# Kernel tuning notes

Hardware: AMD Instinct MI355X
Metric: run time of the kernel (lower is better)

Reference implementation:

```python
import jax, jax.numpy as jnp
import numpy as np

N_ENT = 100000
EMBED_DIM = 128
N_EDGES = 3200000
SPARSE_THRESHOLD = 5


def setup_inputs() -> dict:
    key = jax.random.key(0)
    k1, k2, k3, k4 = jax.random.split(key, 4)
    entity_embeds = jax.random.normal(k1, (N_ENT, EMBED_DIM), dtype=jnp.float32)
    node_degrees = jax.random.randint(k2, (N_ENT,), 0, 40, dtype=jnp.int64)
    path_rows = jnp.sort(jax.random.randint(k3, (N_EDGES,), 0, N_ENT, dtype=jnp.int64))
    path_cols = jax.random.randint(k4, (N_EDGES,), 0, N_ENT, dtype=jnp.int64)
    return {
        "entity_embeds": entity_embeds,
        "node_degrees": node_degrees,
        "path_rows": path_rows,
        "path_cols": path_cols,
    }


def reference(entity_embeds, node_degrees, path_rows, path_cols):
    N, dim = entity_embeds.shape
    # node_edge_count = scatter_add(ones, rows), clamped to >= 1
    ones = jnp.ones(path_rows.shape[0], dtype=entity_embeds.dtype)
    node_edge_count = jax.ops.segment_sum(ones, path_rows, num_segments=N)
    node_edge_count = jnp.clip(node_edge_count, 1.0, None)
    # SpMM: remote[i] = sum over path edges (i -> j) of entity_embeds[j]
    gathered = entity_embeds[path_cols]  # [E, dim] (fused into segment_sum by XLA)
    remote = jax.ops.segment_sum(gathered, path_rows, num_segments=N)
    # degree-normalize then mask to sparse (low-degree) nodes only
    remote = remote / node_edge_count[:, None]
    sparse_mask = (node_degrees <= SPARSE_THRESHOLD).astype(entity_embeds.dtype)
    remote = remote * sparse_mask[:, None]
    return remote
```

## Files before the change

kernel.cpp:

```cpp
#include <hip/hip_runtime.h>

#define N_ENT 100000
#define EMBED_DIM 128
#define SPARSE_THRESHOLD 5
#define N4 (N_ENT * 32)

#define WS_ROWSTART_OFF 64
#define WS_LIST_OFF     100096
#define WS_BF16_OFF_INT 200096
#define WS_NEEDED_BYTES ((size_t)WS_BF16_OFF_INT * 4 + (size_t)N4 * 8)

#define B_ZERO 1408
#define B_CONV 2304
#define B_BND  352
#define B_CMP  32
#define B_TOT  (B_ZERO + B_CONV + B_BND + B_CMP)

__device__ __forceinline__ unsigned short bf16_rne(float f) {
    unsigned int u = __float_as_uint(f);
    u += 0x7FFFu + ((u >> 16) & 1u);
    return (unsigned short)(u >> 16);
}
__device__ __forceinline__ float bf16_up(unsigned short h) {
    return __uint_as_float(((unsigned int)h) << 16);
}

__global__ __launch_bounds__(256) void prep_kernel(
    const float4* __restrict__ emb4,
    const int*    __restrict__ rows,
    const int*    __restrict__ degrees,
    float4*       __restrict__ out4,
    ushort4*      __restrict__ embw,
    int*          __restrict__ row_start,
    int*          __restrict__ sparse_list,
    int*          __restrict__ counter,
    int n_edges)
{
    const int b = blockIdx.x;
    if (b < B_ZERO) {
        const float4 z = make_float4(0.f, 0.f, 0.f, 0.f);
        for (int i = b * 256 + threadIdx.x; i < N4; i += B_ZERO * 256)
            out4[i] = z;
    } else if (b < B_ZERO + B_CONV) {
        for (int i = (b - B_ZERO) * 256 + threadIdx.x; i < N4; i += B_CONV * 256) {
            const float4 v = emb4[i];
            ushort4 o;
            o.x = bf16_rne(v.x); o.y = bf16_rne(v.y);
            o.z = bf16_rne(v.z); o.w = bf16_rne(v.w);
            embw[i] = o;
        }
    } else if (b < B_ZERO + B_CONV + B_BND) {
        const int t  = (b - B_ZERO - B_CONV) * 256 + threadIdx.x;
        const int NT = B_BND * 256;
        const int4* rows4 = (const int4*)rows;
        const int n_quads = n_edges >> 2;
        for (int q = t; q < n_quads; q += NT) {
            const int e0 = q << 2;
            const int4 v = rows4[q];
            int rp = (e0 == 0) ? -1 : rows[e0 - 1];
            const int rv[4] = {v.x, v.y, v.z, v.w};
            #pragma unroll
            for (int k = 0; k < 4; ++k) {
                const int e = e0 + k;
                const int r = rv[k];
                for (int qq = rp + 1; qq <= r; ++qq) row_start[qq] = e;
                if (e == n_edges - 1)
                    for (int qq = r + 1; qq <= N_ENT; ++qq) row_start[qq] = n_edges;
                rp = r;
            }
        }
        for (int e = (n_quads << 2) + t; e < n_edges; e += NT) {
            const int r  = rows[e];
            const int rp = (e == 0) ? -1 : rows[e - 1];
            for (int qq = rp + 1; qq <= r; ++qq) row_start[qq] = e;
            if (e == n_edges - 1)
                for (int qq = r + 1; qq <= N_ENT; ++qq) row_start[qq] = n_edges;
        }
    } else {
        const int t = (b - B_ZERO - B_CONV - B_BND) * 256 + threadIdx.x;
        for (int r = t; r < N_ENT; r += B_CMP * 256) {
            if (degrees[r] <= SPARSE_THRESHOLD)
                sparse_list[atomicAdd(counter, 1)] = r;
        }
    }
}

__global__ __launch_bounds__(256) void agg_sparse_bf16_kernel(
    const ushort4* __restrict__ embw,
    const int*     __restrict__ row_start,
    const int*     __restrict__ cols,
    const int*     __restrict__ sparse_list,
    const int*     __restrict__ counter,
    float4*        __restrict__ out4)
{
    const int nsparse = *counter;
    const int sub  = threadIdx.x >> 5;
    const int lane = threadIdx.x & 31;

    for (int idx = blockIdx.x * 8 + sub; idx < nsparse; idx += gridDim.x * 8) {
        const int row   = sparse_list[idx];
        const int start = row_start[row];
        const int end   = row_start[row + 1];

        float4 acc = make_float4(0.f, 0.f, 0.f, 0.f);
        int e = start;
        for (; e + 8 <= end; e += 8) {
            int c[8];
            #pragma unroll
            for (int k = 0; k < 8; ++k) c[k] = cols[e + k];
            ushort4 v[8];
            #pragma unroll
            for (int k = 0; k < 8; ++k) v[k] = embw[(size_t)c[k] * 32 + lane];
            #pragma unroll
            for (int k = 0; k < 8; ++k) {
                acc.x += bf16_up(v[k].x); acc.y += bf16_up(v[k].y);
                acc.z += bf16_up(v[k].z); acc.w += bf16_up(v[k].w);
            }
        }
        for (; e < end; ++e) {
            const ushort4 v = embw[(size_t)cols[e] * 32 + lane];
            acc.x += bf16_up(v.x); acc.y += bf16_up(v.y);
            acc.z += bf16_up(v.z); acc.w += bf16_up(v.w);
        }

        const int cnt = end - start;
        const float inv = 1.0f / (float)(cnt > 0 ? cnt : 1);
        acc.x *= inv; acc.y *= inv; acc.z *= inv; acc.w *= inv;
        out4[(size_t)row * 32 + lane] = acc;
    }
}

__global__ void seg_bounds_kernel(const int* __restrict__ rows,
                                  int* __restrict__ row_start,
                                  int n_edges) {
    int e = blockIdx.x * blockDim.x + threadIdx.x;
    const int stride = gridDim.x * blockDim.x;
    for (; e < n_edges; e += stride) {
        const int r  = rows[e];
        const int rp = (e == 0) ? -1 : rows[e - 1];
        for (int q = rp + 1; q <= r; ++q) row_start[q] = e;
        if (e == n_edges - 1)
            for (int q = r + 1; q <= N_ENT; ++q) row_start[q] = n_edges;
    }
}

__global__ __launch_bounds__(256) void path_agg_kernel(
    const float4* __restrict__ embeds4,
    const int*    __restrict__ degrees,
    const int*    __restrict__ row_start,
    const int*    __restrict__ cols,
    float4*       __restrict__ out4)
{
    const int sub  = threadIdx.x >> 5;
    const int lane = threadIdx.x & 31;
    const int row  = blockIdx.x * 8 + sub;

    float4* orow = out4 + (size_t)row * 32;
    if (degrees[row] > SPARSE_THRESHOLD) {
        orow[lane] = make_float4(0.f, 0.f, 0.f, 0.f);
        return;
    }
    const int start = row_start[row];
    const int end   = row_start[row + 1];
    float4 acc = make_float4(0.f, 0.f, 0.f, 0.f);
    for (int e = start; e < end; ++e) {
        float4 v = embeds4[(size_t)cols[e] * 32 + lane];
        acc.x += v.x; acc.y += v.y; acc.z += v.z; acc.w += v.w;
    }
    const int cnt = end - start;
    const float inv = 1.0f / (float)(cnt > 0 ? cnt : 1);
    acc.x *= inv; acc.y *= inv; acc.z *= inv; acc.w *= inv;
    orow[lane] = acc;
}

extern "C" void kernel_launch(void* const* d_in, const int* in_sizes, int n_in,
                              void* d_out, int out_size, void* d_ws, size_t ws_size,
                              hipStream_t stream) {
    const float* embeds  = (const float*)d_in[0];
    const int*   degrees = (const int*)d_in[1];
    const int*   rows    = (const int*)d_in[2];
    const int*   cols    = (const int*)d_in[3];
    float* out = (float*)d_out;
    const int n_edges = in_sizes[2];

    if (ws_size >= WS_NEEDED_BYTES) {
        int* wsi         = (int*)d_ws;
        int* counter     = wsi;
        int* row_start   = wsi + WS_ROWSTART_OFF;
        int* sparse_list = wsi + WS_LIST_OFF;
        ushort4* embw    = (ushort4*)(wsi + WS_BF16_OFF_INT);

        hipMemsetAsync(counter, 0, sizeof(int), stream);
        prep_kernel<<<B_TOT, 256, 0, stream>>>(
            (const float4*)embeds, rows, degrees, (float4*)out, embw,
            row_start, sparse_list, counter, n_edges);
        agg_sparse_bf16_kernel<<<2048, 256, 0, stream>>>(
            embw, row_start, cols, sparse_list, counter, (float4*)out);
    } else if (ws_size >= (size_t)(N_ENT + 1) * sizeof(int)) {
        int* row_start = (int*)d_ws;
        seg_bounds_kernel<<<1024, 256, 0, stream>>>(rows, row_start, n_edges);
        path_agg_kernel<<<N_ENT / 8, 256, 0, stream>>>(
            (const float4*)embeds, degrees, row_start, cols, (float4*)out);
    }
}
```

Before: 160.1 us.

## Unify prep roles across all threads and zero only dense rows with nontemporal stores

New measurement: 159.9 us. About the same (-0.1%).

```diff
diff --git a/kernel.cpp b/kernel.cpp
--- a/kernel.cpp
+++ b/kernel.cpp
@@ -10,11 +10,10 @@
 #define WS_BF16_OFF_INT 200096
 #define WS_NEEDED_BYTES ((size_t)WS_BF16_OFF_INT * 4 + (size_t)N4 * 8)
 
-#define B_ZERO 1408
-#define B_CONV 2304
-#define B_BND  352
-#define B_CMP  32
-#define B_TOT  (B_ZERO + B_CONV + B_BND + B_CMP)
+#define PREP_BLOCKS 2048
+#define AGG_BLOCKS  2048
+
+typedef float nfloat4 __attribute__((ext_vector_type(4)));
 
 __device__ __forceinline__ unsigned short bf16_rne(float f) {
     unsigned int u = __float_as_uint(f);
@@ -36,25 +35,25 @@
     int*          __restrict__ counter,
     int n_edges)
 {
-    const int b = blockIdx.x;
-    if (b < B_ZERO) {
-        const float4 z = make_float4(0.f, 0.f, 0.f, 0.f);
-        for (int i = b * 256 + threadIdx.x; i < N4; i += B_ZERO * 256)
-            out4[i] = z;
-    } else if (b < B_ZERO + B_CONV) {
-        for (int i = (b - B_ZERO) * 256 + threadIdx.x; i < N4; i += B_CONV * 256) {
-            const float4 v = emb4[i];
-            ushort4 o;
-            o.x = bf16_rne(v.x); o.y = bf16_rne(v.y);
-            o.z = bf16_rne(v.z); o.w = bf16_rne(v.w);
-            embw[i] = o;
-        }
-    } else if (b < B_ZERO + B_CONV + B_BND) {
-        const int t  = (b - B_ZERO - B_CONV) * 256 + threadIdx.x;
-        const int NT = B_BND * 256;
+    const int tid = blockIdx.x * 256 + threadIdx.x;
+    const int NT  = PREP_BLOCKS * 256;
+
+    const nfloat4 z = {0.f, 0.f, 0.f, 0.f};
+    nfloat4* outn = (nfloat4*)out4;
+    for (int i = tid; i < N4; i += NT) {
+        const float4 v = emb4[i];
+        ushort4 o;
+        o.x = bf16_rne(v.x); o.y = bf16_rne(v.y);
+        o.z = bf16_rne(v.z); o.w = bf16_rne(v.w);
+        embw[i] = o;
+        if (degrees[i >> 5] > SPARSE_THRESHOLD)
+            __builtin_nontemporal_store(z, &outn[i]);
+    }
+
+    {
         const int4* rows4 = (const int4*)rows;
         const int n_quads = n_edges >> 2;
-        for (int q = t; q < n_quads; q += NT) {
+        for (int q = tid; q < n_quads; q += NT) {
             const int e0 = q << 2;
             const int4 v = rows4[q];
             int rp = (e0 == 0) ? -1 : rows[e0 - 1];
@@ -69,19 +68,18 @@
                 rp = r;
             }
         }
-        for (int e = (n_quads << 2) + t; e < n_edges; e += NT) {
+        for (int e = (n_quads << 2) + tid; e < n_edges; e += NT) {
             const int r  = rows[e];
             const int rp = (e == 0) ? -1 : rows[e - 1];
             for (int qq = rp + 1; qq <= r; ++qq) row_start[qq] = e;
             if (e == n_edges - 1)
                 for (int qq = r + 1; qq <= N_ENT; ++qq) row_start[qq] = n_edges;
         }
-    } else {
-        const int t = (b - B_ZERO - B_CONV - B_BND) * 256 + threadIdx.x;
-        for (int r = t; r < N_ENT; r += B_CMP * 256) {
-            if (degrees[r] <= SPARSE_THRESHOLD)
-                sparse_list[atomicAdd(counter, 1)] = r;
-        }
+    }
+
+    for (int r = tid; r < N_ENT; r += NT) {
+        if (degrees[r] <= SPARSE_THRESHOLD)
+            sparse_list[atomicAdd(counter, 1)] = r;
     }
 }
 
@@ -190,11 +188,11 @@
         int* sparse_list = wsi + WS_LIST_OFF;
         ushort4* embw    = (ushort4*)(wsi + WS_BF16_OFF_INT);
 
-        hipMemsetAsync(counter, 0, sizeof(int), stream);
-        prep_kernel<<<B_TOT, 256, 0, stream>>>(
+        (void)hipMemsetAsync(counter, 0, sizeof(int), stream);
+        prep_kernel<<<PREP_BLOCKS, 256, 0, stream>>>(
             (const float4*)embeds, rows, degrees, (float4*)out, embw,
             row_start, sparse_list, counter, n_edges);
-        agg_sparse_bf16_kernel<<<2048, 256, 0, stream>>>(
+        agg_sparse_bf16_kernel<<<AGG_BLOCKS, 256, 0, stream>>>(
             embw, row_start, cols, sparse_list, counter, (float4*)out);
     } else if (ws_size >= (size_t)(N_ENT + 1) * sizeof(int)) {
         int* row_start = (int*)d_ws;
```
